# Kernel tuning notes

Measured on AMD Instinct MI355X. Metric: run time of the kernel, lower is better.

Reference implementation:

```python
import jax, jax.numpy as jnp
import numpy as np

TEMP = 0.1
EPS = 1e-9  # torch CosineSimilarity eps


def setup_inputs() -> dict:
    key = jax.random.key(0)
    k1, k2 = jax.random.split(key)
    h = jax.random.normal(k1, (16384, 2048), dtype=jnp.float32)
    W = jax.random.normal(k2, (512, 2048), dtype=jnp.float32) * (1.0 / np.sqrt(2048))
    return {"h": h, "W": W}


def reference(h, W):
    # process_reps: h already 2D -> identity. Split into anchor / context halves.
    B = h.shape[0] // 2
    wz = h[:B] @ W.T      # [B, low_rank_dim]
    wc = h[B:] @ W.T      # [B, low_rank_dim]

    # CosineSimilarity(dim=-1, eps=1e-9): dot / max(||z||*||c||, eps), pairwise BxB
    nz = jnp.linalg.norm(wz, axis=-1)  # [B]
    nc = jnp.linalg.norm(wc, axis=-1)  # [B]
    sim = (wz @ wc.T) / jnp.maximum(nz[:, None] * nc[None, :], EPS)  # [B, B]
    sim = sim / TEMP

    sim_mean = sim.mean()
    sim_pos = jnp.diagonal(sim).mean()
    logprob = -jax.nn.log_softmax(sim, axis=1)
    loss = jnp.diagonal(logprob).mean()
    # matches loss_dict entries: {'loss', 'loss_pos', 'loss_neg'}
    return jnp.stack([loss, sim_pos, sim_mean])
```

## Files before the change

### kernel.cpp

```cpp
#include <hip/hip_runtime.h>


typedef __attribute__((ext_vector_type(8))) short bf16x8;
typedef __attribute__((ext_vector_type(4))) float floatx4;
typedef unsigned char uchar;

__device__ __forceinline__ unsigned short f2bf(float f) {
    union { float f; unsigned u; } v; v.f = f;
    unsigned r = (v.u + 0x7FFFu + ((v.u >> 16) & 1u)) >> 16;
    return (unsigned short)r;
}

__device__ __forceinline__ void async_copy16(const void* g, void* l) {
    __builtin_amdgcn_global_load_lds(
        (const __attribute__((address_space(1))) void*)g,
        (__attribute__((address_space(3))) void*)l,
        16, 0, 0);
}

__global__ __launch_bounds__(256) void cast_fp8_kernel(
    const float* __restrict__ src, uchar* __restrict__ dst, int n, float scale)
{
    const int i = (blockIdx.x * 256 + threadIdx.x) * 8;
    if (i + 7 < n) {
        float4 a = *reinterpret_cast<const float4*>(src + i);
        float4 b = *reinterpret_cast<const float4*>(src + i + 4);
        const int p01 = __builtin_amdgcn_cvt_pk_fp8_f32(a.x * scale, a.y * scale, 0, 0);
        const int p23 = __builtin_amdgcn_cvt_pk_fp8_f32(a.z * scale, a.w * scale, 0, 0);
        const int p45 = __builtin_amdgcn_cvt_pk_fp8_f32(b.x * scale, b.y * scale, 0, 0);
        const int p67 = __builtin_amdgcn_cvt_pk_fp8_f32(b.z * scale, b.w * scale, 0, 0);
        int2 w;
        w.x = (p01 & 0xffff) | (p23 << 16);
        w.y = (p45 & 0xffff) | (p67 << 16);
        *reinterpret_cast<int2*>(dst + i) = w;
    }
}

__device__ __forceinline__ size_t fl_off(int row_g, int col_g) {
    const int g = row_g >> 4, r15 = row_g & 15;
    const int c = col_g >> 5, q = (col_g >> 3) & 3, b = col_g & 7;
    return ((size_t)g * 16 + c) * 512 + (size_t)(q * 16 + r15) * 8 + b;
}

__global__ __launch_bounds__(256) void g1_main(
    const uchar* __restrict__ h8, const uchar* __restrict__ W8,
    uchar* __restrict__ Z8F, float* __restrict__ norm2)
{
    __shared__ __align__(16) uchar As[128 * 64];
    __shared__ __align__(16) uchar Bs[128 * 64];

    const int o = blockIdx.y * 4 + blockIdx.x;
    const int xcd = o & 7, idx = o >> 3;
    const int bn = idx & 3;
    const int bm = xcd * 16 + (idx >> 2);
    const int t = threadIdx.x;
    const int wave = t >> 6, lane = t & 63;
    const int wm = wave & 1, wn = wave >> 1;
    const int quad = lane >> 4, l15 = lane & 15;

    floatx4 acc[4][4];
    #pragma unroll
    for (int i = 0; i < 4; i++)
        #pragma unroll
        for (int j = 0; j < 4; j++) acc[i][j] = {0.f, 0.f, 0.f, 0.f};

    const int srow0 = wave * 32 + (lane >> 2);
    const int srow1 = srow0 + 16;
    const int p = lane & 3;
    const int sw0 = (p ^ ((srow0 >> 1) & 3)) << 4;
    const int sw1 = (p ^ ((srow1 >> 1) & 3)) << 4;
    const uchar* gA0 = h8 + (size_t)(bm * 128 + srow0) * 2048 + sw0;
    const uchar* gA1 = h8 + (size_t)(bm * 128 + srow1) * 2048 + sw1;
    const uchar* gB0 = W8 + (size_t)(bn * 128 + srow0) * 2048 + sw0;
    const uchar* gB1 = W8 + (size_t)(bn * 128 + srow1) * 2048 + sw1;
    uchar* lA0 = &As[(wave * 32 +  0) * 64];
    uchar* lA1 = &As[(wave * 32 + 16) * 64];
    uchar* lB0 = &Bs[(wave * 32 +  0) * 64];
    uchar* lB1 = &Bs[(wave * 32 + 16) * 64];

    for (int k0 = 0; k0 < 2048; k0 += 64) {
        async_copy16(gA0 + k0, lA0);
        async_copy16(gA1 + k0, lA1);
        async_copy16(gB0 + k0, lB0);
        async_copy16(gB1 + k0, lB1);
        __syncthreads();
        #pragma unroll
        for (int ch = 0; ch < 2; ch++) {
            const int s = ch * 2 + (quad >> 1);
            const int sub = (quad & 1) * 8;
            long a[4], b[4];
            #pragma unroll
            for (int i = 0; i < 4; i++) {
                const int row = wm * 64 + i * 16 + l15;
                a[i] = *reinterpret_cast<const long*>(
                    &As[row * 64 + ((s ^ ((row >> 1) & 3)) << 4) + sub]);
            }
            #pragma unroll
            for (int j = 0; j < 4; j++) {
                const int row = wn * 64 + j * 16 + l15;
                b[j] = *reinterpret_cast<const long*>(
                    &Bs[row * 64 + ((s ^ ((row >> 1) & 3)) << 4) + sub]);
            }
            #pragma unroll
            for (int i = 0; i < 4; i++)
                #pragma unroll
                for (int j = 0; j < 4; j++)
                    acc[i][j] = __builtin_amdgcn_mfma_f32_16x16x32_fp8_fp8(
                        a[i], b[j], acc[i][j], 0, 0, 0);
        }
        __syncthreads();
    }

    #pragma unroll
    for (int i = 0; i < 4; i++) {
        #pragma unroll
        for (int r = 0; r < 4; r++) {
            const int row_g = bm * 128 + wm * 64 + i * 16 + quad * 4 + r;
            const int pk01 = __builtin_amdgcn_cvt_pk_fp8_f32(acc[i][0][r], acc[i][1][r], 0, 0);
            const int pk23 = __builtin_amdgcn_cvt_pk_fp8_f32(acc[i][2][r], acc[i][3][r], 0, 0);
            const uchar q8[4] = { (uchar)(pk01 & 0xff), (uchar)((pk01 >> 8) & 0xff),
                                  (uchar)(pk23 & 0xff), (uchar)((pk23 >> 8) & 0xff) };
            #pragma unroll
            for (int j = 0; j < 4; j++) {
                const int col_g = bn * 128 + wn * 64 + j * 16 + l15;
                Z8F[fl_off(row_g, col_g)] = q8[j];
            }
            const float q0 = __builtin_amdgcn_cvt_f32_fp8(pk01, 0);
            const float q1 = __builtin_amdgcn_cvt_f32_fp8(pk01, 1);
            const float q2 = __builtin_amdgcn_cvt_f32_fp8(pk23, 0);
            const float q3 = __builtin_amdgcn_cvt_f32_fp8(pk23, 1);
            float pw = q0 * q0 + q1 * q1 + q2 * q2 + q3 * q3;
            pw += __shfl_xor(pw, 1, 16);
            pw += __shfl_xor(pw, 2, 16);
            pw += __shfl_xor(pw, 4, 16);
            pw += __shfl_xor(pw, 8, 16);
            if (l15 == 0) atomicAdd(&norm2[row_g], pw);
        }
    }
}

__global__ __launch_bounds__(256) void g1_slow(
    const float* __restrict__ h, const float* __restrict__ W,
    uchar* __restrict__ Z8F, float* __restrict__ norm2)
{
    __shared__ __align__(16) unsigned short As[128][40];
    __shared__ __align__(16) unsigned short Bs[128][40];

    const int bn = blockIdx.x, bm = blockIdx.y;
    const int t = threadIdx.x;
    const int wave = t >> 6, lane = t & 63;
    const int wm = wave & 1, wn = wave >> 1;
    const int quad = lane >> 4, l15 = lane & 15;

    floatx4 acc[4][4];
    #pragma unroll
    for (int i = 0; i < 4; i++)
        #pragma unroll
        for (int j = 0; j < 4; j++) acc[i][j] = {0.f, 0.f, 0.f, 0.f};

    const int lrow = t >> 1, lhalf = t & 1;
    const float* ga = h + (size_t)(bm * 128 + lrow) * 2048 + lhalf * 16;
    const float* gb = W + (size_t)(bn * 128 + lrow) * 2048 + lhalf * 16;

    for (int k0 = 0; k0 < 2048; k0 += 32) {
        #pragma unroll
        for (int c = 0; c < 4; c++) {
            const float4 va = *reinterpret_cast<const float4*>(ga + k0 + c * 4);
            const float4 vb = *reinterpret_cast<const float4*>(gb + k0 + c * 4);
            ushort4 ua = make_ushort4(f2bf(va.x), f2bf(va.y), f2bf(va.z), f2bf(va.w));
            ushort4 ub = make_ushort4(f2bf(vb.x), f2bf(vb.y), f2bf(vb.z), f2bf(vb.w));
            *reinterpret_cast<ushort4*>(&As[lrow][lhalf * 16 + c * 4]) = ua;
            *reinterpret_cast<ushort4*>(&Bs[lrow][lhalf * 16 + c * 4]) = ub;
        }
        __syncthreads();
        bf16x8 af[4], bfr[4];
        #pragma unroll
        for (int i = 0; i < 4; i++)
            af[i] = *reinterpret_cast<const bf16x8*>(&As[wm * 64 + i * 16 + l15][quad * 8]);
        #pragma unroll
        for (int j = 0; j < 4; j++)
            bfr[j] = *reinterpret_cast<const bf16x8*>(&Bs[wn * 64 + j * 16 + l15][quad * 8]);
        #pragma unroll
        for (int i = 0; i < 4; i++)
            #pragma unroll
            for (int j = 0; j < 4; j++)
                acc[i][j] = __builtin_amdgcn_mfma_f32_16x16x32_bf16(af[i], bfr[j], acc[i][j], 0, 0, 0);
        __syncthreads();
    }

    #pragma unroll
    for (int i = 0; i < 4; i++) {
        #pragma unroll
        for (int r = 0; r < 4; r++) {
            const int row_g = bm * 128 + wm * 64 + i * 16 + quad * 4 + r;
            const int pk01 = __builtin_amdgcn_cvt_pk_fp8_f32(acc[i][0][r], acc[i][1][r], 0, 0);
            const int pk23 = __builtin_amdgcn_cvt_pk_fp8_f32(acc[i][2][r], acc[i][3][r], 0, 0);
            const uchar q8[4] = { (uchar)(pk01 & 0xff), (uchar)((pk01 >> 8) & 0xff),
                                  (uchar)(pk23 & 0xff), (uchar)((pk23 >> 8) & 0xff) };
            #pragma unroll
            for (int j = 0; j < 4; j++) {
                const int col_g = bn * 128 + wn * 64 + j * 16 + l15;
                Z8F[fl_off(row_g, col_g)] = q8[j];
            }
            const float q0 = __builtin_amdgcn_cvt_f32_fp8(pk01, 0);
            const float q1 = __builtin_amdgcn_cvt_f32_fp8(pk01, 1);
            const float q2 = __builtin_amdgcn_cvt_f32_fp8(pk23, 0);
            const float q3 = __builtin_amdgcn_cvt_f32_fp8(pk23, 1);
            float pw = q0 * q0 + q1 * q1 + q2 * q2 + q3 * q3;
            pw += __shfl_xor(pw, 1, 16);
            pw += __shfl_xor(pw, 2, 16);
            pw += __shfl_xor(pw, 4, 16);
            pw += __shfl_xor(pw, 8, 16);
            if (l15 == 0) atomicAdd(&norm2[row_g], pw);
        }
    }
}

__global__ __launch_bounds__(256, 4) void g2_main(
    const uchar* __restrict__ Z8F, const float* __restrict__ norm2,
    float* __restrict__ rowse, float* __restrict__ bsum, float* __restrict__ bdiag)
{
    __shared__ __align__(16) uchar Bs[32768];
    __shared__ float red[8];
    float (*lds_red)[20] = (float (*)[20])(void*)Bs;

    const int o = blockIdx.y * 64 + blockIdx.x;
    const int xcd = o & 7, idx = o >> 3;
    const int bg = idx >> 7, r = idx & 127;
    const int bm = xcd * 8 + (r >> 4);
    const int bn = bg * 16 + (r & 15);
    const int t = threadIdx.x;
    const int wave = t >> 6, lane = t & 63;
    const int quad = lane >> 4, l15 = lane & 15;

    const uchar* gB = Z8F + (size_t)(512 + bn * 8) * 8192 + t * 16;
    #pragma unroll
    for (int s = 0; s < 8; s++)
        async_copy16(gB + s * 8192, &Bs[s * 4096 + wave * 1024]);

    floatx4 acc[2][8];
    #pragma unroll
    for (int i = 0; i < 2; i++)
        #pragma unroll
        for (int j = 0; j < 8; j++) acc[i][j] = {0.f, 0.f, 0.f, 0.f};

    const uchar* baseA = Z8F + (size_t)(bm * 8 + wave * 2) * 8192 + lane * 8;

    long ab[3][2];
    #pragma unroll
    for (int d = 0; d < 2; d++)
        #pragma unroll
        for (int i = 0; i < 2; i++)
            ab[d][i] = *reinterpret_cast<const long*>(baseA + i * 8192 + d * 512);

    __syncthreads();

    #pragma unroll
    for (int c = 0; c < 16; c++) {
        const int cl = c & 7;
        if (c < 14) {
            #pragma unroll
            for (int i = 0; i < 2; i++)
                ab[(c + 2) % 3][i] = *reinterpret_cast<const long*>(
                    baseA + i * 8192 + (c + 2) * 512);
        }
        long bb[8];
        #pragma unroll
        for (int j = 0; j < 8; j++)
            bb[j] = *reinterpret_cast<const long*>(&Bs[j * 4096 + cl * 512 + lane * 8]);
        __builtin_amdgcn_s_setprio(1);
        #pragma unroll
        for (int i = 0; i < 2; i++)
            #pragma unroll
            for (int j = 0; j < 8; j++)
                acc[i][j] = __builtin_amdgcn_mfma_f32_16x16x32_fp8_fp8(
                    ab[c % 3][i], bb[j], acc[i][j], 0, 0, 0);
        __builtin_amdgcn_s_setprio(0);
        if (c == 7) {
            __syncthreads();
            #pragma unroll
            for (int s = 0; s < 8; s++)
                async_copy16(gB + s * 8192 + 4096, &Bs[s * 4096 + wave * 1024]);
            __syncthreads();
        }
    }

    __syncthreads();

    float rc8[8];
    #pragma unroll
    for (int j = 0; j < 8; j++)
        rc8[j] = rsqrtf(fmaxf(norm2[8192 + bn * 128 + j * 16 + l15], 1e-30f));

    const bool diagblk = (bm == bn);
    float s_tot2 = 0.f, s_diag2 = 0.f;
    #pragma unroll
    for (int i = 0; i < 2; i++) {
        #pragma unroll
        for (int rr = 0; rr < 4; rr++) {
            const int row_t = wave * 32 + i * 16 + quad * 4 + rr;
            const float rzl2 = rsqrtf(fmaxf(norm2[bm * 128 + row_t], 1e-30f)) * 14.4269504089f;
            float rx = 0.f;
            #pragma unroll
            for (int j = 0; j < 8; j++) {
                const float sim2 = acc[i][j][rr] * rzl2 * rc8[j];
                s_tot2 += sim2;
                rx += exp2f(sim2);
                if (diagblk && j == wave * 2 + i && l15 == quad * 4 + rr)
                    s_diag2 += sim2;
            }
            lds_red[row_t][l15] = rx;
        }
    }
    __syncthreads();

    {
        const int row = t >> 1, half = t & 1;
        float v = 0.f;
        #pragma unroll
        for (int cc = 0; cc < 8; cc++) v += lds_red[row][half * 8 + cc];
        v += __shfl_xor(v, 1, 64);
        if (half == 0) atomicAdd(&rowse[bm * 128 + row], v);
    }

    #pragma unroll
    for (int off = 32; off; off >>= 1) {
        s_tot2  += __shfl_xor(s_tot2, off, 64);
        s_diag2 += __shfl_xor(s_diag2, off, 64);
    }
    if (lane == 0) { red[wave] = s_tot2; red[4 + wave] = s_diag2; }
    __syncthreads();
    if (t == 0) {
        bsum[bm * 64 + bn]  = (red[0] + red[1] + red[2] + red[3]) * 0.69314718056f;
        bdiag[bm * 64 + bn] = (red[4] + red[5] + red[6] + red[7]) * 0.69314718056f;
    }
}

__global__ __launch_bounds__(256) void finalize_kernel(
    const float* __restrict__ rowse, const float* __restrict__ bsum,
    const float* __restrict__ bdiag, float* __restrict__ out)
{
    float a = 0.f, b = 0.f, c = 0.f;
    for (int i = threadIdx.x; i < 8192; i += 256) a += logf(rowse[i]);
    for (int i = threadIdx.x; i < 4096; i += 256) { b += bsum[i]; c += bdiag[i]; }
    #pragma unroll
    for (int off = 32; off; off >>= 1) {
        a += __shfl_xor(a, off, 64);
        b += __shfl_xor(b, off, 64);
        c += __shfl_xor(c, off, 64);
    }
    __shared__ float ra[4], rb[4], rc[4];
    const int wave = threadIdx.x >> 6, lane = threadIdx.x & 63;
    if (lane == 0) { ra[wave] = a; rb[wave] = b; rc[wave] = c; }
    __syncthreads();
    if (threadIdx.x == 0) {
        const float A = ra[0] + ra[1] + ra[2] + ra[3];
        const float B = rb[0] + rb[1] + rb[2] + rb[3];
        const float C = rc[0] + rc[1] + rc[2] + rc[3];
        const float diag_mean = C / 8192.f;
        out[0] = A / 8192.f - diag_mean;
        out[1] = diag_mean;
        out[2] = B / (8192.f * 8192.f);
    }
}

extern "C" void kernel_launch(void* const* d_in, const int* in_sizes, int n_in,
                              void* d_out, int out_size, void* d_ws, size_t ws_size,
                              hipStream_t stream) {
    const float* h = (const float*)d_in[0];
    const float* W = (const float*)d_in[1];
    float* out = (float*)d_out;

    char* ws = (char*)d_ws;
    float* norm2 = (float*)(ws);
    float* rowse = (float*)(ws + 65536);
    float* bsum  = (float*)(ws + 98304);
    float* bdiag = (float*)(ws + 114688);
    uchar* Z8F   = (uchar*)(ws + 131072);
    uchar* W8    = (uchar*)(ws + 8519680);
    uchar* h8    = (uchar*)(ws + 9568256);
    const size_t NEED_FAST = 43122688ull;

    hipMemsetAsync(ws, 0, 131072, stream);

    if (ws_size >= NEED_FAST) {
        const int nh = 16384 * 2048, nw = 512 * 2048;
        hipLaunchKernelGGL(cast_fp8_kernel, dim3(nh / 2048), dim3(256), 0, stream, h, h8, nh, 1.0f);
        hipLaunchKernelGGL(cast_fp8_kernel, dim3(nw / 2048), dim3(256), 0, stream, W, W8, nw, 32.0f);
        hipLaunchKernelGGL(g1_main, dim3(4, 128), dim3(256), 0, stream, h8, W8, Z8F, norm2);
    } else {
        hipLaunchKernelGGL(g1_slow, dim3(4, 128), dim3(256), 0, stream, h, W, Z8F, norm2);
    }
    hipLaunchKernelGGL(g2_main, dim3(64, 64), dim3(256), 0, stream, Z8F, norm2, rowse, bsum, bdiag);
    hipLaunchKernelGGL(finalize_kernel, dim3(1), dim3(256), 0, stream, rowse, bsum, bdiag, out);
}
```

Baseline: 291.7 us.

## Fuse h fp8 cast into projection GEMM with full-width N tile

Removes the separate cast pass over h (128 MB fp32 read plus a 32 MB fp8 write and re-read). The projection kernel now loads fp32 h directly, converts it to fp8 in registers and writes it to LDS, prefetching the next k-slice during the MFMA work. Each block covers 64 rows and all 512 output columns, so h is read once and the norm is written directly rather than through atomics. The cost is 128 accumulator registers per thread, only 256 blocks on the device, and W8 reloaded by every block.

New measurement: 285.2 us. -2.2%, faster.

```diff
diff --git a/kernel.cpp b/kernel.cpp
--- a/kernel.cpp
+++ b/kernel.cpp
@@ -42,17 +42,123 @@
     return ((size_t)g * 16 + c) * 512 + (size_t)(q * 16 + r15) * 8 + b;
 }
 
-__global__ __launch_bounds__(256) void g1_main(
-    const uchar* __restrict__ h8, const uchar* __restrict__ W8,
+__global__ __launch_bounds__(256, 2) void g1f(
+    const float* __restrict__ h, const uchar* __restrict__ W8,
     uchar* __restrict__ Z8F, float* __restrict__ norm2)
 {
-    __shared__ __align__(16) uchar As[128 * 64];
-    __shared__ __align__(16) uchar Bs[128 * 64];
-
-    const int o = blockIdx.y * 4 + blockIdx.x;
-    const int xcd = o & 7, idx = o >> 3;
-    const int bn = idx & 3;
-    const int bm = xcd * 16 + (idx >> 2);
+    __shared__ __align__(16) uchar As[64 * 64];
+    __shared__ __align__(16) uchar Bs[512 * 64];
+
+    const int blk = blockIdx.x;
+    const int t = threadIdx.x;
+    const int wave = t >> 6, lane = t & 63;
+    const int quad = lane >> 4, l15 = lane & 15;
+
+    floatx4 acc[32];
+    #pragma unroll
+    for (int j = 0; j < 32; j++) acc[j] = {0.f, 0.f, 0.f, 0.f};
+
+    const int arow = t >> 2, ap = t & 3;
+    const float* gH = h + (size_t)(blk * 64 + arow) * 2048 + ap * 16;
+    uchar* lA = &As[arow * 64 + ((ap ^ ((arow >> 1) & 3)) << 4)];
+
+    const int brow0 = wave * 128 + (lane >> 2);
+    const int bswz = ((lane & 3) ^ ((brow0 >> 1) & 3)) << 4;
+    const uchar* gB = W8 + (size_t)brow0 * 2048 + bswz;
+    uchar* lB = &Bs[wave * 128 * 64];
+
+    const int swzr = (l15 >> 1) & 3;
+    const int arow_r = wave * 16 + l15;
+
+    float4 f0 = *reinterpret_cast<const float4*>(gH + 0);
+    float4 f1 = *reinterpret_cast<const float4*>(gH + 4);
+    float4 f2 = *reinterpret_cast<const float4*>(gH + 8);
+    float4 f3 = *reinterpret_cast<const float4*>(gH + 12);
+
+    for (int k0 = 0; k0 < 2048; k0 += 64) {
+        #pragma unroll
+        for (int s = 0; s < 8; s++)
+            async_copy16(gB + k0 + s * 32768, lB + s * 1024);
+        {
+            const int p01 = __builtin_amdgcn_cvt_pk_fp8_f32(f0.x, f0.y, 0, 0);
+            const int p23 = __builtin_amdgcn_cvt_pk_fp8_f32(f0.z, f0.w, 0, 0);
+            const int p45 = __builtin_amdgcn_cvt_pk_fp8_f32(f1.x, f1.y, 0, 0);
+            const int p67 = __builtin_amdgcn_cvt_pk_fp8_f32(f1.z, f1.w, 0, 0);
+            const int p89 = __builtin_amdgcn_cvt_pk_fp8_f32(f2.x, f2.y, 0, 0);
+            const int pAB = __builtin_amdgcn_cvt_pk_fp8_f32(f2.z, f2.w, 0, 0);
+            const int pCD = __builtin_amdgcn_cvt_pk_fp8_f32(f3.x, f3.y, 0, 0);
+            const int pEF = __builtin_amdgcn_cvt_pk_fp8_f32(f3.z, f3.w, 0, 0);
+            int4 pk;
+            pk.x = (p01 & 0xffff) | (p23 << 16);
+            pk.y = (p45 & 0xffff) | (p67 << 16);
+            pk.z = (p89 & 0xffff) | (pAB << 16);
+            pk.w = (pCD & 0xffff) | (pEF << 16);
+            *reinterpret_cast<int4*>(lA) = pk;
+        }
+        __syncthreads();
+
+        if (k0 < 2048 - 64) {
+            f0 = *reinterpret_cast<const float4*>(gH + k0 + 64);
+            f1 = *reinterpret_cast<const float4*>(gH + k0 + 68);
+            f2 = *reinterpret_cast<const float4*>(gH + k0 + 72);
+            f3 = *reinterpret_cast<const float4*>(gH + k0 + 76);
+        }
+
+        #pragma unroll
+        for (int ch = 0; ch < 2; ch++) {
+            const int s = ch * 2 + (quad >> 1);
+            const int sub = (quad & 1) * 8;
+            const int phys = ((s ^ swzr) << 4) + sub;
+            const long a = *reinterpret_cast<const long*>(&As[arow_r * 64 + phys]);
+            #pragma unroll
+            for (int jg = 0; jg < 4; jg++) {
+                long bb[8];
+                #pragma unroll
+                for (int u = 0; u < 8; u++) {
+                    const int brow = (jg * 8 + u) * 16 + l15;
+                    bb[u] = *reinterpret_cast<const long*>(&Bs[brow * 64 + phys]);
+                }
+                __builtin_amdgcn_s_setprio(1);
+                #pragma unroll
+                for (int u = 0; u < 8; u++)
+                    acc[jg * 8 + u] = __builtin_amdgcn_mfma_f32_16x16x32_fp8_fp8(
+                        a, bb[u], acc[jg * 8 + u], 0, 0, 0);
+                __builtin_amdgcn_s_setprio(0);
+            }
+        }
+        __syncthreads();
+    }
+
+    #pragma unroll
+    for (int r = 0; r < 4; r++) {
+        const int row_g = blk * 64 + wave * 16 + quad * 4 + r;
+        float pw = 0.f;
+        #pragma unroll
+        for (int jp = 0; jp < 16; jp++) {
+            const int pk = __builtin_amdgcn_cvt_pk_fp8_f32(
+                acc[2 * jp][r], acc[2 * jp + 1][r], 0, 0);
+            Z8F[fl_off(row_g, (2 * jp) * 16 + l15)]     = (uchar)(pk & 0xff);
+            Z8F[fl_off(row_g, (2 * jp + 1) * 16 + l15)] = (uchar)((pk >> 8) & 0xff);
+            const float q0 = __builtin_amdgcn_cvt_f32_fp8(pk, 0);
+            const float q1 = __builtin_amdgcn_cvt_f32_fp8(pk, 1);
+            pw += q0 * q0 + q1 * q1;
+        }
+        pw += __shfl_xor(pw, 1, 16);
+        pw += __shfl_xor(pw, 2, 16);
+        pw += __shfl_xor(pw, 4, 16);
+        pw += __shfl_xor(pw, 8, 16);
+        if (l15 == 0) norm2[row_g] = pw;
+    }
+}
+
+__global__ __launch_bounds__(256) void g1_slow(
+    const float* __restrict__ h, const float* __restrict__ W,
+    uchar* __restrict__ Z8F, float* __restrict__ norm2)
+{
+    __shared__ __align__(16) unsigned short As[128][40];
+    __shared__ __align__(16) unsigned short Bs[128][40];
+
+    const int bn = blockIdx.x, bm = blockIdx.y;
     const int t = threadIdx.x;
     const int wave = t >> 6, lane = t & 63;
     const int wm = wave & 1, wn = wave >> 1;
@@ -64,50 +170,33 @@
         #pragma unroll
         for (int j = 0; j < 4; j++) acc[i][j] = {0.f, 0.f, 0.f, 0.f};
 
-    const int srow0 = wave * 32 + (lane >> 2);
-    const int srow1 = srow0 + 16;
-    const int p = lane & 3;
-    const int sw0 = (p ^ ((srow0 >> 1) & 3)) << 4;
-    const int sw1 = (p ^ ((srow1 >> 1) & 3)) << 4;
-    const uchar* gA0 = h8 + (size_t)(bm * 128 + srow0) * 2048 + sw0;
-    const uchar* gA1 = h8 + (size_t)(bm * 128 + srow1) * 2048 + sw1;
-    const uchar* gB0 = W8 + (size_t)(bn * 128 + srow0) * 2048 + sw0;
-    const uchar* gB1 = W8 + (size_t)(bn * 128 + srow1) * 2048 + sw1;
-    uchar* lA0 = &As[(wave * 32 +  0) * 64];
-    uchar* lA1 = &As[(wave * 32 + 16) * 64];
-    uchar* lB0 = &Bs[(wave * 32 +  0) * 64];
-    uchar* lB1 = &Bs[(wave * 32 + 16) * 64];
-
-    for (int k0 = 0; k0 < 2048; k0 += 64) {
-        async_copy16(gA0 + k0, lA0);
-        async_copy16(gA1 + k0, lA1);
-        async_copy16(gB0 + k0, lB0);
-        async_copy16(gB1 + k0, lB1);
+    const int lrow = t >> 1, lhalf = t & 1;
+    const float* ga = h + (size_t)(bm * 128 + lrow) * 2048 + lhalf * 16;
+    const float* gb = W + (size_t)(bn * 128 + lrow) * 2048 + lhalf * 16;
+
+    for (int k0 = 0; k0 < 2048; k0 += 32) {
+        #pragma unroll
+        for (int c = 0; c < 4; c++) {
+            const float4 va = *reinterpret_cast<const float4*>(ga + k0 + c * 4);
+            const float4 vb = *reinterpret_cast<const float4*>(gb + k0 + c * 4);
+            ushort4 ua = make_ushort4(f2bf(va.x), f2bf(va.y), f2bf(va.z), f2bf(va.w));
+            ushort4 ub = make_ushort4(f2bf(vb.x), f2bf(vb.y), f2bf(vb.z), f2bf(vb.w));
+            *reinterpret_cast<ushort4*>(&As[lrow][lhalf * 16 + c * 4]) = ua;
+            *reinterpret_cast<ushort4*>(&Bs[lrow][lhalf * 16 + c * 4]) = ub;
+        }
         __syncthreads();
-        #pragma unroll
-        for (int ch = 0; ch < 2; ch++) {
-            const int s = ch * 2 + (quad >> 1);
-            const int sub = (quad & 1) * 8;
-            long a[4], b[4];
-            #pragma unroll
-            for (int i = 0; i < 4; i++) {
-                const int row = wm * 64 + i * 16 + l15;
-                a[i] = *reinterpret_cast<const long*>(
-                    &As[row * 64 + ((s ^ ((row >> 1) & 3)) << 4) + sub]);
-            }
-            #pragma unroll
-            for (int j = 0; j < 4; j++) {
-                const int row = wn * 64 + j * 16 + l15;
-                b[j] = *reinterpret_cast<const long*>(
-                    &Bs[row * 64 + ((s ^ ((row >> 1) & 3)) << 4) + sub]);
-            }
-            #pragma unroll
-            for (int i = 0; i < 4; i++)
-                #pragma unroll
-                for (int j = 0; j < 4; j++)
-                    acc[i][j] = __builtin_amdgcn_mfma_f32_16x16x32_fp8_fp8(
-                        a[i], b[j], acc[i][j], 0, 0, 0);
-        }
+        bf16x8 af[4], bfr[4];
+        #pragma unroll
+        for (int i = 0; i < 4; i++)
+            af[i] = *reinterpret_cast<const bf16x8*>(&As[wm * 64 + i * 16 + l15][quad * 8]);
+        #pragma unroll
+        for (int j = 0; j < 4; j++)
+            bfr[j] = *reinterpret_cast<const bf16x8*>(&Bs[wn * 64 + j * 16 + l15][quad * 8]);
+        #pragma unroll
+        for (int i = 0; i < 4; i++)
+            #pragma unroll
+            for (int j = 0; j < 4; j++)
+                acc[i][j] = __builtin_amdgcn_mfma_f32_16x16x32_bf16(af[i], bfr[j], acc[i][j], 0, 0, 0);
         __syncthreads();
     }
 
@@ -139,83 +228,6 @@
     }
 }
 
-__global__ __launch_bounds__(256) void g1_slow(
-    const float* __restrict__ h, const float* __restrict__ W,
-    uchar* __restrict__ Z8F, float* __restrict__ norm2)
-{
-    __shared__ __align__(16) unsigned short As[128][40];
-    __shared__ __align__(16) unsigned short Bs[128][40];
-
-    const int bn = blockIdx.x, bm = blockIdx.y;
-    const int t = threadIdx.x;
-    const int wave = t >> 6, lane = t & 63;
-    const int wm = wave & 1, wn = wave >> 1;
-    const int quad = lane >> 4, l15 = lane & 15;
-
-    floatx4 acc[4][4];
-    #pragma unroll
-    for (int i = 0; i < 4; i++)
-        #pragma unroll
-        for (int j = 0; j < 4; j++) acc[i][j] = {0.f, 0.f, 0.f, 0.f};
-
-    const int lrow = t >> 1, lhalf = t & 1;
-    const float* ga = h + (size_t)(bm * 128 + lrow) * 2048 + lhalf * 16;
-    const float* gb = W + (size_t)(bn * 128 + lrow) * 2048 + lhalf * 16;
-
-    for (int k0 = 0; k0 < 2048; k0 += 32) {
-        #pragma unroll
-        for (int c = 0; c < 4; c++) {
-            const float4 va = *reinterpret_cast<const float4*>(ga + k0 + c * 4);
-            const float4 vb = *reinterpret_cast<const float4*>(gb + k0 + c * 4);
-            ushort4 ua = make_ushort4(f2bf(va.x), f2bf(va.y), f2bf(va.z), f2bf(va.w));
-            ushort4 ub = make_ushort4(f2bf(vb.x), f2bf(vb.y), f2bf(vb.z), f2bf(vb.w));
-            *reinterpret_cast<ushort4*>(&As[lrow][lhalf * 16 + c * 4]) = ua;
-            *reinterpret_cast<ushort4*>(&Bs[lrow][lhalf * 16 + c * 4]) = ub;
-        }
-        __syncthreads();
-        bf16x8 af[4], bfr[4];
-        #pragma unroll
-        for (int i = 0; i < 4; i++)
-            af[i] = *reinterpret_cast<const bf16x8*>(&As[wm * 64 + i * 16 + l15][quad * 8]);
-        #pragma unroll
-        for (int j = 0; j < 4; j++)
-            bfr[j] = *reinterpret_cast<const bf16x8*>(&Bs[wn * 64 + j * 16 + l15][quad * 8]);
-        #pragma unroll
-        for (int i = 0; i < 4; i++)
-            #pragma unroll
-            for (int j = 0; j < 4; j++)
-                acc[i][j] = __builtin_amdgcn_mfma_f32_16x16x32_bf16(af[i], bfr[j], acc[i][j], 0, 0, 0);
-        __syncthreads();
-    }
-
-    #pragma unroll
-    for (int i = 0; i < 4; i++) {
-        #pragma unroll
-        for (int r = 0; r < 4; r++) {
-            const int row_g = bm * 128 + wm * 64 + i * 16 + quad * 4 + r;
-            const int pk01 = __builtin_amdgcn_cvt_pk_fp8_f32(acc[i][0][r], acc[i][1][r], 0, 0);
-            const int pk23 = __builtin_amdgcn_cvt_pk_fp8_f32(acc[i][2][r], acc[i][3][r], 0, 0);
-            const uchar q8[4] = { (uchar)(pk01 & 0xff), (uchar)((pk01 >> 8) & 0xff),
-                                  (uchar)(pk23 & 0xff), (uchar)((pk23 >> 8) & 0xff) };
-            #pragma unroll
-            for (int j = 0; j < 4; j++) {
-                const int col_g = bn * 128 + wn * 64 + j * 16 + l15;
-                Z8F[fl_off(row_g, col_g)] = q8[j];
-            }
-            const float q0 = __builtin_amdgcn_cvt_f32_fp8(pk01, 0);
-            const float q1 = __builtin_amdgcn_cvt_f32_fp8(pk01, 1);
-            const float q2 = __builtin_amdgcn_cvt_f32_fp8(pk23, 0);
-            const float q3 = __builtin_amdgcn_cvt_f32_fp8(pk23, 1);
-            float pw = q0 * q0 + q1 * q1 + q2 * q2 + q3 * q3;
-            pw += __shfl_xor(pw, 1, 16);
-            pw += __shfl_xor(pw, 2, 16);
-            pw += __shfl_xor(pw, 4, 16);
-            pw += __shfl_xor(pw, 8, 16);
-            if (l15 == 0) atomicAdd(&norm2[row_g], pw);
-        }
-    }
-}
-
 __global__ __launch_bounds__(256, 4) void g2_main(
     const uchar* __restrict__ Z8F, const float* __restrict__ norm2,
     float* __restrict__ rowse, float* __restrict__ bsum, float* __restrict__ bdiag)
@@ -378,16 +390,14 @@
     float* bdiag = (float*)(ws + 114688);
     uchar* Z8F   = (uchar*)(ws + 131072);
     uchar* W8    = (uchar*)(ws + 8519680);
-    uchar* h8    = (uchar*)(ws + 9568256);
-    const size_t NEED_FAST = 43122688ull;
+    const size_t NEED_FAST = 9568256ull;
 
     hipMemsetAsync(ws, 0, 131072, stream);
 
     if (ws_size >= NEED_FAST) {
-        const int nh = 16384 * 2048, nw = 512 * 2048;
-        hipLaunchKernelGGL(cast_fp8_kernel, dim3(nh / 2048), dim3(256), 0, stream, h, h8, nh, 1.0f);
+        const int nw = 512 * 2048;
         hipLaunchKernelGGL(cast_fp8_kernel, dim3(nw / 2048), dim3(256), 0, stream, W, W8, nw, 32.0f);
-        hipLaunchKernelGGL(g1_main, dim3(4, 128), dim3(256), 0, stream, h8, W8, Z8F, norm2);
+        hipLaunchKernelGGL(g1f, dim3(256), dim3(256), 0, stream, h, W8, Z8F, norm2);
     } else {
         hipLaunchKernelGGL(g1_slow, dim3(4, 128), dim3(256), 0, stream, h, W, Z8F, norm2);
     }
```
